# Optimization experiments

Measured on AMD Instinct MI355X. Metric: run time of the kernel, lower is better.

The kernel has to match this reference:

```python
import jax, jax.numpy as jnp
import numpy as np

N_QUBITS = 10
N_LAYERS = 2

# ---- batched statevector simulator helpers (state shape: (B,) + (2,)*n) ----

def _apply1q(state, w, mat):
    # mat: [2,2] complex, same for all batch elements
    s = jnp.moveaxis(state, w + 1, 1)
    s = jnp.einsum('ij,bj...->bi...', mat, s)
    return jnp.moveaxis(s, 1, w + 1)

def _apply1q_b(state, w, mats):
    # mats: [B,2,2] complex, per-batch gate (input-encoding RY)
    s = jnp.moveaxis(state, w + 1, 1)
    s = jnp.einsum('bij,bj...->bi...', mats, s)
    return jnp.moveaxis(s, 1, w + 1)

def _cnot(state, c, t):
    s = jnp.moveaxis(state, (c + 1, t + 1), (1, 2))  # [B,2(ctrl),2(tgt),...]
    s = jnp.concatenate([s[:, :1], jnp.flip(s[:, 1:2], axis=2)], axis=1)
    return jnp.moveaxis(s, (1, 2), (c + 1, t + 1))

def _rz(t):
    p = jnp.exp(-0.5j * t.astype(jnp.complex64))
    z = jnp.zeros((), jnp.complex64)
    return jnp.stack([jnp.stack([p, z]), jnp.stack([z, jnp.conj(p)])])

def _rx(t):
    h = 0.5 * t
    c = jnp.cos(h).astype(jnp.complex64)
    s = jnp.sin(h).astype(jnp.complex64) * (-1j)
    return jnp.stack([jnp.stack([c, s]), jnp.stack([s, c])])

def _ry(t):
    h = 0.5 * t
    c, s = jnp.cos(h), jnp.sin(h)
    return jnp.stack([jnp.stack([c, -s]), jnp.stack([s, c])]).astype(jnp.complex64)

def qlayer(angles, qparams):
    """angles: [B, n_qubits] float -> [B, n_qubits] PauliZ expectations."""
    B = angles.shape[0]
    n = N_QUBITS
    state = jnp.zeros((B,) + (2,) * n, jnp.complex64)
    state = state.at[(slice(None),) + (0,) * n].set(1.0)
    # data-encoding RY with per-batch angles
    half = 0.5 * angles
    c, s = jnp.cos(half), jnp.sin(half)
    for w in range(n):
        row0 = jnp.stack([c[:, w], -s[:, w]], -1)
        row1 = jnp.stack([s[:, w], c[:, w]], -1)
        mats = jnp.stack([row0, row1], 1).astype(jnp.complex64)  # [B,2,2]
        state = _apply1q_b(state, w, mats)
    for l in range(N_LAYERS):
        for w in range(n):
            state = _apply1q(state, w, _rz(qparams[l, w, 0]))
            state = _apply1q(state, w, _rx(qparams[l, w, 1]))
            state = _apply1q(state, w, _ry(qparams[l, w, 2]))
        for w in range(n - 1):
            state = _cnot(state, w, w + 1)
        state = _cnot(state, n - 1, 0)
    probs = jnp.real(state * jnp.conj(state))
    exps = []
    for w in range(n):
        axes = tuple(a for a in range(1, n + 1) if a != w + 1)
        p = jnp.sum(probs, axis=axes)  # [B,2]
        exps.append(p[:, 0] - p[:, 1])
    return jnp.stack(exps, -1)


def setup_inputs() -> dict:
    key = jax.random.key(0)
    ks = jax.random.split(key, 12)
    T, B, D, H = 64, 256, 32, N_QUBITS
    in_dim = D + H
    std = 1.0 / np.sqrt(in_dim)
    inputs = jax.random.normal(ks[0], (T, B, D), jnp.float32)
    qparams = 0.01 * jax.random.normal(ks[1], (N_LAYERS, N_QUBITS, 3), jnp.float32)
    def lin(k1, k2):
        W = jax.random.uniform(k1, (H, in_dim), jnp.float32, -std, std)
        b = jax.random.uniform(k2, (H,), jnp.float32, -std, std)
        return W, b
    W_f, b_f = lin(ks[2], ks[3])
    W_i, b_i = lin(ks[4], ks[5])
    W_g, b_g = lin(ks[6], ks[7])
    W_o, b_o = lin(ks[8], ks[9])
    return dict(inputs=inputs, qparams=qparams, W_f=W_f, b_f=b_f, W_i=W_i, b_i=b_i,
                W_g=W_g, b_g=b_g, W_o=W_o, b_o=b_o)


def reference(inputs, qparams, W_f, b_f, W_i, b_i, W_g, b_g, W_o, b_o):
    T, B, D = inputs.shape
    H = N_QUBITS

    def step(carry, x):
        hx, cx = carry
        comb = jnp.concatenate([x, hx], axis=1)  # [B, D+H]
        pre = jnp.concatenate([
            comb @ W_f.T + b_f,
            comb @ W_i.T + b_i,
            comb @ W_g.T + b_g,
            comb @ W_o.T + b_o,
        ], axis=0)  # [4B, H] -- one fused circuit call for all 4 gates
        q = qlayer(pre, qparams).reshape(4, B, H)
        f = jax.nn.sigmoid(q[0])
        i = jax.nn.sigmoid(q[1])
        g = jnp.tanh(q[2])
        o = jax.nn.sigmoid(q[3])
        cx2 = f * cx + i * g
        hx2 = o * jnp.tanh(cx2)
        return (hx2, cx2), hx2

    hx = jnp.zeros((B, H), jnp.float32)
    cx = jnp.zeros((B, H), jnp.float32)
    (hx, cx), outputs = jax.lax.scan(jax.checkpoint(step), (hx, cx), inputs)
    return outputs, hx, cx
```

## Files before the change

### kernel.cpp

```cpp
#include <hip/hip_runtime.h>

#define TS 64
#define NB 256
#define DI 32
#define NH 10
#define IND 42

typedef float f32x2 __attribute__((ext_vector_type(2)));

#define PKOP2(name, instr, mods) \
__device__ __forceinline__ f32x2 name(f32x2 a, f32x2 b){ \
  f32x2 d; asm(instr " %0, %1, %2 " mods : "=v"(d) : "v"(a), "v"(b)); return d; }
#define PKOP3(name, mods) \
__device__ __forceinline__ f32x2 name(f32x2 a, f32x2 b, f32x2 c){ \
  f32x2 d; asm("v_pk_fma_f32 %0, %1, %2, %3 " mods : "=v"(d) : "v"(a), "v"(b), "v"(c)); return d; }

PKOP2(pk_mul,       "v_pk_mul_f32", "op_sel:[0,0] op_sel_hi:[1,1]")
PKOP2(pk_mul_s0hi,  "v_pk_mul_f32", "op_sel:[1,0] op_sel_hi:[1,1]")
PKOP2(pk_mul_s0lo,  "v_pk_mul_f32", "op_sel:[0,0] op_sel_hi:[0,1]")
PKOP2(pk_mul_s1lo,  "v_pk_mul_f32", "op_sel:[0,0] op_sel_hi:[1,0]")
PKOP2(pk_addsub_ll, "v_pk_add_f32", "op_sel:[0,0] op_sel_hi:[0,0] neg_hi:[0,1]")
PKOP2(pk_addsub_lh, "v_pk_add_f32", "op_sel:[0,1] op_sel_hi:[0,1] neg_hi:[0,1]")
PKOP3(pk_fma_s1lo,  "op_sel:[0,0,0] op_sel_hi:[1,0,1]")
PKOP3(pk_fma_s1hi,  "op_sel:[0,1,0] op_sel_hi:[1,1,1]")
PKOP3(pk_fma_s1swap,"op_sel:[0,1,0] op_sel_hi:[1,0,1]")
PKOP3(pk_fma_am,    "op_sel:[1,1,0] op_sel_hi:[1,0,1] neg_lo:[1,0,0]")
PKOP3(pk_fma_s0lo,  "op_sel:[0,0,0] op_sel_hi:[0,1,1]")
PKOP3(pk_fma_s0hi,  "op_sel:[1,0,0] op_sel_hi:[1,1,1]")

template<int CTRL>
__device__ __forceinline__ float dppx(float v){
  return __int_as_float(__builtin_amdgcn_update_dpp(
      0, __float_as_int(v), CTRL, 0xF, 0xF, true));
}
__device__ __forceinline__ float rl(float v, int lane){
  return __int_as_float(__builtin_amdgcn_readlane(__float_as_int(v), lane));
}
__device__ __forceinline__ f32x2 rl2(f32x2 v, int lane){
  f32x2 r; r.x = rl(v.x, lane); r.y = rl(v.y, lane); return r;
}
__device__ __forceinline__ void pin(float& x){ asm volatile("" : "+v"(x)); }
__device__ __forceinline__ void pinv(f32x2& x){ asm volatile("" : "+v"(x)); }

__device__ __forceinline__ float tanhr(float x){ float e = __expf(2.f*x); return 1.f - 2.f/(e + 1.f); }

__device__ __forceinline__ void mkU(float t1, float t2, float t3, float* dst){
  float c1 = __cosf(0.5f*t1), s1 = __sinf(0.5f*t1);
  float c2 = __cosf(0.5f*t2), s2 = __sinf(0.5f*t2);
  float c3 = __cosf(0.5f*t3), s3 = __sinf(0.5f*t3);
  float A00r =  c2*c1, A00i = -c2*s1;
  float A01r =  s2*s1, A01i = -s2*c1;
  float A10r = -s2*s1, A10i = -s2*c1;
  float A11r =  c2*c1, A11i =  c2*s1;
  dst[0] = c3*A00r - s3*A10r; dst[1] = c3*A00i - s3*A10i;
  dst[2] = c3*A01r - s3*A11r; dst[3] = c3*A01i - s3*A11i;
  dst[4] = s3*A00r + c3*A10r; dst[5] = s3*A00i + c3*A10i;
  dst[6] = s3*A01r + c3*A11r; dst[7] = s3*A01i + c3*A11i;
}

__device__ __forceinline__ float3 qf(float q00, float q11, float q01){
  return make_float3(0.5f*(q00+q11), 0.5f*(q00-q11), 0.5f*q01);
}

__global__ __launch_bounds__(256) __attribute__((amdgpu_waves_per_eu(1, 1)))
void qlstm_kernel(const float* __restrict__ xin,
                  const float* __restrict__ qp,
                  const float* __restrict__ Wf, const float* __restrict__ bfp,
                  const float* __restrict__ Wi, const float* __restrict__ bip,
                  const float* __restrict__ Wg, const float* __restrict__ bgp,
                  const float* __restrict__ Wo, const float* __restrict__ bop,
                  float* __restrict__ out)
{
  __shared__ float lx[TS][DI + 1];
  __shared__ float lwx[4][TS][NH];
  __shared__ __align__(16) float lBw[4][NH][4];
  __shared__ __align__(16) float lq[2][NH][4];
  __shared__ float lhout[TS][NH];

  const int tid  = threadIdx.x;
  const int b    = blockIdx.x;
  const int g    = tid >> 6;
  const int lane = tid & 63;
  const int hq   = lane >> 2;
  const int sg   = lane & 3;
  const int hrow = (lane < NH) ? lane : 0;

  const float* Wsel = (g==0) ? Wf : (g==1) ? Wi : (g==2) ? Wg : Wo;
  const float* bsel = (g==0) ? bfp : (g==1) ? bip : (g==2) ? bgp : bop;

  for (int i = tid; i < TS*DI; i += 256) {
    int tt = i >> 5, d = i & 31;
    lx[tt][d] = xin[(size_t)tt*(NB*DI) + b*DI + d];
  }
  if (lane < NH) {
    float u[8];
    mkU(qp[30 + lane*3 + 0], qp[30 + lane*3 + 1], qp[30 + lane*3 + 2], u);
    float B00 = u[0]*u[0]+u[1]*u[1] - (u[4]*u[4]+u[5]*u[5]);
    float B11 = u[2]*u[2]+u[3]*u[3] - (u[6]*u[6]+u[7]*u[7]);
    float B01r= u[0]*u[2]+u[1]*u[3] - (u[4]*u[6]+u[5]*u[7]);
    float B01i= u[1]*u[2]-u[0]*u[3] - (u[5]*u[6]-u[4]*u[7]);
    *reinterpret_cast<float4*>(&lBw[g][lane][0]) = make_float4(B00,B11,B01r,B01i);
  }
  __syncthreads();

  {
    float acc[NH];
    #pragma unroll
    for (int h = 0; h < NH; h++) acc[h] = bsel[h];
    #pragma unroll
    for (int k = 0; k < DI; k++) {
      float xk = lx[lane][k];
      #pragma unroll
      for (int h = 0; h < NH; h++) acc[h] = fmaf(Wsel[h*IND + k], xk, acc[h]);
    }
    #pragma unroll
    for (int h = 0; h < NH; h++) lwx[g][lane][h] = acc[h];
  }

  float wh[NH];
  #pragma unroll
  for (int j = 0; j < NH; j++) wh[j] = Wsel[hrow*IND + DI + j];

  float3 Qn0, Qn1, Qer, Qei;
  {
    float U1[8];
    mkU(qp[hrow*3+0], qp[hrow*3+1], qp[hrow*3+2], U1);
    float r00r=U1[0], r00i=U1[1], r01r=U1[2], r01i=U1[3];
    float r10r=U1[4], r10i=U1[5], r11r=U1[6], r11i=U1[7];
    float P0r,P0i,P1r,P1i, R0r,R0i,R1r,R1i;
    if (lane == 0) {
      P0r=r00r; P0i=r00i; P1r=r01r; P1i=r01i;
      R0r=r10r; R0i=r10i; R1r=r11r; R1i=r11i;
    } else {
      P0r=0.5f*(r00r+r10r); P0i=0.5f*(r00i+r10i);
      P1r=0.5f*(r01r+r11r); P1i=0.5f*(r01i+r11i);
      R0r=0.5f*(r00r-r10r); R0i=0.5f*(r00i-r10i);
      R1r=0.5f*(r01r-r11r); R1i=0.5f*(r01i-r11i);
    }
    Qn0 = qf(P0r*P0r+P0i*P0i, P1r*P1r+P1i*P1i, 2.f*(P0r*P1r+P0i*P1i));
    Qn1 = qf(R0r*R0r+R0i*R0i, R1r*R1r+R1i*R1i, 2.f*(R0r*R1r+R0i*R1i));
    Qer = qf(R0r*P0r+R0i*P0i, R1r*P1r+R1i*P1i,
             (R0r*P1r+R0i*P1i) + (R1r*P0r+R1i*P0i));
    Qei = qf(R0i*P0r-R0r*P0i, R1i*P1r-R1r*P1i,
             (R0i*P1r-R0r*P1i) + (R1i*P0r-R1r*P0i));
  }
  f32x2 QnA, QnB, QnG, QeA, QeB, QeG;
  QnA.x=Qn0.x; QnA.y=Qn1.x;  QnB.x=Qn0.y; QnB.y=Qn1.y;  QnG.x=Qn0.z; QnG.y=Qn1.z;
  QeA.x=Qer.x; QeA.y=Qei.x;  QeB.x=Qer.y; QeB.y=Qei.y;  QeG.x=Qer.z; QeG.y=Qei.z;

  float4 b0 = *reinterpret_cast<const float4*>(&lBw[g][0][0]);
  if (hq == 0) b0 = make_float4(1.f, 1.f, 0.f, 0.f);
  float k0, k3, ka, kb;
  if      (sg == 0) { k0 = b0.x;  k3 = b0.y;  ka = b0.z; kb = -b0.w; }
  else if (sg == 1) { k0 = b0.z;  k3 = b0.z;  ka = 0.5f*(b0.x + b0.y); kb = 0.f; }
  else if (sg == 2) { k0 = -b0.w; k3 = b0.w;  ka = 0.f;  kb = 0.5f*(b0.y - b0.x); }
  else              { k0 = b0.y;  k3 = b0.x;  ka = b0.z; kb = b0.w; }
  {
    const float gsc = (sg == 0 || sg == 3) ? 0.5f : 1.0f;
    k0 *= gsc; k3 *= gsc; ka *= gsc; kb *= gsc;
  }
  const float ka2 = ka + ka, kb2 = kb + kb;
  f32x2 KA, KB, KC, KD;
  KA.x = k0;   KA.y = k0;
  KB.x = k3;   KB.y = -k3;
  KC.x = ka2;  KC.y = -ka2;
  KD.x = -kb2; KD.y = -kb2;

  f32x2 K1[9], K2[9], K3[9], K4[9];
  #pragma unroll
  for (int w = 1; w <= 9; w++) {
    float4 bb = *reinterpret_cast<const float4*>(&lBw[g][w][0]);
    bool inM = (hq == 0) || (w <= hq);
    float Cp = inM ? (bb.x + bb.y) : 2.f;
    float Cm = inM ? (bb.x - bb.y) : 0.f;
    float Cr2 = inM ? (bb.z + bb.z) : 0.f;
    float Ci2 = inM ? (bb.w + bb.w) : 0.f;
    K1[w-1].x = Cp;        K1[w-1].y = Cm;
    K2[w-1].x = Cm + Cm;   K2[w-1].y = Cp + Cp;
    K3[w-1].x = Cr2;       K3[w-1].y = Ci2;
    K4[w-1].x = -(Ci2+Ci2); K4[w-1].y = Cr2 + Cr2;
  }

  #pragma unroll
  for (int w = 0; w < 9; w++) { pinv(K1[w]); pinv(K2[w]); pinv(K3[w]); pinv(K4[w]); }
  #pragma unroll
  for (int j = 0; j < NH; j++) pin(wh[j]);
  pinv(QnA); pinv(QnB); pinv(QnG); pinv(QeA); pinv(QeB); pinv(QeG);
  pinv(KA); pinv(KB); pinv(KC); pinv(KD);

  const float se = (g == 2) ? -2.f : -1.f;
  const float sa = (g == 2) ?  2.f :  1.f;
  const float sb = (g == 2) ? -1.f :  0.f;

  float cstate = 0.f, hval = 0.f;
  float wxcur = lwx[g][0][hrow];

  for (int t = 0; t < TS; t++) {
    const int tb = t & 1;

    float h0 = rl(hval,0), h1 = rl(hval,1), h2 = rl(hval,2), h3 = rl(hval,3), h4 = rl(hval,4);
    float h5 = rl(hval,5), h6 = rl(hval,6), h7 = rl(hval,7), h8 = rl(hval,8), h9 = rl(hval,9);
    float p0 = fmaf(wh[1], h1, wh[0]*h0);
    float p1 = fmaf(wh[3], h3, wh[2]*h2);
    float p2 = fmaf(wh[5], h5, wh[4]*h4);
    float p3 = fmaf(wh[7], h7, wh[6]*h6);
    float p4 = fmaf(wh[9], h9, wh[8]*h8);
    float pre = wxcur + ((p0 + p1) + (p2 + p3) + p4);

    wxcur = lwx[g][(t+1) & (TS-1)][hrow];

    float th = pre * 0.15915494309189535f;
    f32x2 CS; CS.x = __builtin_amdgcn_cosf(th); CS.y = __builtin_amdgcn_sinf(th);
    f32x2 NP = pk_fma_s1lo(QnB, CS, pk_fma_s1hi(QnG, CS, QnA));
    f32x2 EP = pk_fma_s1lo(QeB, CS, pk_fma_s1hi(QeG, CS, QeA));

    f32x2 V1 = rl2(NP, 0), V2 = rl2(EP, 0);
    f32x2 P1 = pk_fma_s1hi(KB, V1, pk_mul_s1lo(KA, V1));
    f32x2 P2 = pk_fma_s1swap(KD, V2, pk_mul(KC, V2));
    #pragma unroll
    for (int w = 1; w <= 9; w++) {
      f32x2 W1 = rl2(NP, w), W2 = rl2(EP, w);
      f32x2 U  = pk_addsub_ll(P1, P2);
      f32x2 M  = pk_mul(U, W1);
      f32x2 T1 = pk_mul_s0hi(P1, W2);
      f32x2 AB = pk_fma_am(P2, W2, T1);
      f32x2 QS = pk_addsub_lh(M, M);
      f32x2 T2 = pk_mul_s0lo(QS, K1[w-1]);
      P1 = pk_fma_s0lo(AB, K2[w-1], T2);
      f32x2 T3 = pk_mul_s0hi(QS, K3[w-1]);
      P2 = pk_fma_s0hi(AB, K4[w-1], T3);
    }

    float Qv = P1.x, Sv = P1.y, Av = P2.x, Bv = P2.y;
    float QpS = Qv + Sv;
    float QmS = Qv - Sv;
    float t0 = (sg & 1) ? Av  : QpS;
    float t1 = (sg & 1) ? QmS : Bv;
    float Ee = (sg & 2) ? t1 : t0;
    Ee += dppx<0xB1>(Ee);
    Ee += dppx<0x4E>(Ee);
    if ((lane & 3) == 0 && hq < NH) {
      lq[tb][hq][g] = fmaf(sa, 1.f/(1.f + __expf(se*Ee)), sb);
    }
    __syncthreads();

    float4 gates = *reinterpret_cast<const float4*>(&lq[tb][hrow][0]);
    cstate = gates.x*cstate + gates.y*gates.z;
    hval = gates.w*tanhr(cstate);
    if (g == 0 && lane < NH) lhout[t][lane] = hval;
  }

  __syncthreads();
  for (int i = tid; i < TS*NH; i += 256) {
    int tt = i / NH, h = i - tt*NH;
    out[(size_t)tt*(NB*NH) + b*NH + h] = lhout[tt][h];
  }
  if (g == 0 && lane < NH) {
    out[(size_t)TS*NB*NH + b*NH + lane]          = hval;
    out[(size_t)TS*NB*NH + NB*NH + b*NH + lane]  = cstate;
  }
}

extern "C" void kernel_launch(void* const* d_in, const int* in_sizes, int n_in,
                              void* d_out, int out_size, void* d_ws, size_t ws_size,
                              hipStream_t stream) {
  (void)in_sizes; (void)n_in; (void)d_ws; (void)ws_size; (void)out_size;
  qlstm_kernel<<<dim3(NB), dim3(256), 0, stream>>>(
      (const float*)d_in[0], (const float*)d_in[1],
      (const float*)d_in[2], (const float*)d_in[3],
      (const float*)d_in[4], (const float*)d_in[5],
      (const float*)d_in[6], (const float*)d_in[7],
      (const float*)d_in[8], (const float*)d_in[9],
      (float*)d_out);
}
```

Before: 118.2 us.

## Collapse block to single wavefront, one lane per gate-qubit, drop barriers

The block shrinks from four wavefronts (one per gate) to a single 64-lane wavefront in which each 16-lane group handles one gate and each lane one qubit. Per-wire values are exchanged through LDS instead of readlane. Each lane now evaluates all four observable components with two interleaved packed chains, which removes the DPP reduction and the per-step __syncthreads. The x-projection for all four gates runs in each thread before the time loop. The aim is to cut per-step barrier and cross-wave synchronisation latency on the serial recurrence, at the cost of more ALU work per lane and reliance on intra-wave LDS ordering without explicit barriers.

```diff
diff --git a/kernel.cpp b/kernel.cpp
--- a/kernel.cpp
+++ b/kernel.cpp
@@ -15,29 +15,18 @@
 __device__ __forceinline__ f32x2 name(f32x2 a, f32x2 b, f32x2 c){ \
   f32x2 d; asm("v_pk_fma_f32 %0, %1, %2, %3 " mods : "=v"(d) : "v"(a), "v"(b), "v"(c)); return d; }
 
-PKOP2(pk_mul,       "v_pk_mul_f32", "op_sel:[0,0] op_sel_hi:[1,1]")
-PKOP2(pk_mul_s0hi,  "v_pk_mul_f32", "op_sel:[1,0] op_sel_hi:[1,1]")
-PKOP2(pk_mul_s0lo,  "v_pk_mul_f32", "op_sel:[0,0] op_sel_hi:[0,1]")
-PKOP2(pk_mul_s1lo,  "v_pk_mul_f32", "op_sel:[0,0] op_sel_hi:[1,0]")
-PKOP2(pk_addsub_ll, "v_pk_add_f32", "op_sel:[0,0] op_sel_hi:[0,0] neg_hi:[0,1]")
-PKOP2(pk_addsub_lh, "v_pk_add_f32", "op_sel:[0,1] op_sel_hi:[0,1] neg_hi:[0,1]")
-PKOP3(pk_fma_s1lo,  "op_sel:[0,0,0] op_sel_hi:[1,0,1]")
-PKOP3(pk_fma_s1hi,  "op_sel:[0,1,0] op_sel_hi:[1,1,1]")
-PKOP3(pk_fma_s1swap,"op_sel:[0,1,0] op_sel_hi:[1,0,1]")
-PKOP3(pk_fma_am,    "op_sel:[1,1,0] op_sel_hi:[1,0,1] neg_lo:[1,0,0]")
-PKOP3(pk_fma_s0lo,  "op_sel:[0,0,0] op_sel_hi:[0,1,1]")
-PKOP3(pk_fma_s0hi,  "op_sel:[1,0,0] op_sel_hi:[1,1,1]")
-
-template<int CTRL>
-__device__ __forceinline__ float dppx(float v){
-  return __int_as_float(__builtin_amdgcn_update_dpp(
-      0, __float_as_int(v), CTRL, 0xF, 0xF, true));
-}
+PKOP2(pk_add_p,   "v_pk_add_f32", "op_sel:[0,0] op_sel_hi:[1,1]")
+PKOP2(pk_sub_p,   "v_pk_add_f32", "op_sel:[0,0] op_sel_hi:[1,1] neg_lo:[0,1] neg_hi:[0,1]")
+PKOP2(pk_mul_bl,  "v_pk_mul_f32", "op_sel:[0,0] op_sel_hi:[1,0]")
+PKOP2(pk_mul_bh,  "v_pk_mul_f32", "op_sel:[0,1] op_sel_hi:[1,1]")
+PKOP2(pk_mul_bl_na,"v_pk_mul_f32","op_sel:[0,0] op_sel_hi:[1,0] neg_lo:[1,0] neg_hi:[1,0]")
+PKOP3(pk_fma_bl,  "op_sel:[0,0,0] op_sel_hi:[1,0,1]")
+PKOP3(pk_fma_bh,  "op_sel:[0,1,0] op_sel_hi:[1,1,1]")
+PKOP3(pk_fma_bh_na,"op_sel:[0,1,0] op_sel_hi:[1,1,1] neg_lo:[1,0,0] neg_hi:[1,0,0]")
+PKOP3(pk_fma_bl_nac,"op_sel:[0,0,0] op_sel_hi:[1,0,1] neg_lo:[1,0,1] neg_hi:[1,0,1]")
+
 __device__ __forceinline__ float rl(float v, int lane){
   return __int_as_float(__builtin_amdgcn_readlane(__float_as_int(v), lane));
-}
-__device__ __forceinline__ f32x2 rl2(f32x2 v, int lane){
-  f32x2 r; r.x = rl(v.x, lane); r.y = rl(v.y, lane); return r;
 }
 __device__ __forceinline__ void pin(float& x){ asm volatile("" : "+v"(x)); }
 __device__ __forceinline__ void pinv(f32x2& x){ asm volatile("" : "+v"(x)); }
@@ -62,7 +51,31 @@
   return make_float3(0.5f*(q00+q11), 0.5f*(q00-q11), 0.5f*q01);
 }
 
-__global__ __launch_bounds__(256) __attribute__((amdgpu_waves_per_eu(1, 1)))
+__device__ __forceinline__ void wire_step(f32x2& Q, f32x2& S, f32x2& A, f32x2& B,
+                                          f32x2 W1, f32x2 W2,
+                                          f32x2 K1w, f32x2 K3w, f32x2 K5w){
+  f32x2 u0 = pk_add_p(Q, A);
+  f32x2 u3 = pk_sub_p(Q, A);
+  f32x2 m0 = pk_mul_bl(u0, W1);
+  f32x2 m3 = pk_mul_bh(u3, W1);
+  f32x2 t1 = pk_mul_bl(S, W2);
+  f32x2 am = pk_fma_bh_na(B, W2, t1);
+  f32x2 t2 = pk_mul_bh(S, W2);
+  f32x2 bm = pk_fma_bl(B, W2, t2);
+  f32x2 q2 = pk_add_p(m0, m3);
+  f32x2 s2 = pk_sub_p(m0, m3);
+  f32x2 am2 = pk_add_p(am, am);
+  f32x2 t3 = pk_mul_bl(q2, K1w);
+  Q = pk_fma_bh(am2, K1w, t3);
+  f32x2 t4 = pk_mul_bh(q2, K1w);
+  S = pk_fma_bl(am2, K1w, t4);
+  f32x2 t5 = pk_mul_bl_na(bm, K5w);
+  A = pk_fma_bl(s2, K3w, t5);
+  f32x2 t6 = pk_mul_bh(bm, K5w);
+  B = pk_fma_bh(s2, K3w, t6);
+}
+
+__global__ __launch_bounds__(64) __attribute__((amdgpu_waves_per_eu(1, 1)))
 void qlstm_kernel(const float* __restrict__ xin,
                   const float* __restrict__ qp,
                   const float* __restrict__ Wf, const float* __restrict__ bfp,
@@ -73,48 +86,48 @@
 {
   __shared__ float lx[TS][DI + 1];
   __shared__ float lwx[4][TS][NH];
-  __shared__ __align__(16) float lBw[4][NH][4];
-  __shared__ __align__(16) float lq[2][NH][4];
+  __shared__ __align__(16) float lBw[NH][4];
+  __shared__ __align__(16) float4 lvv[4][17];
+  __shared__ __align__(16) float lact[16][4];
   __shared__ float lhout[TS][NH];
 
   const int tid  = threadIdx.x;
   const int b    = blockIdx.x;
-  const int g    = tid >> 6;
-  const int lane = tid & 63;
-  const int hq   = lane >> 2;
-  const int sg   = lane & 3;
-  const int hrow = (lane < NH) ? lane : 0;
+  const int g    = tid >> 4;
+  const int hq   = tid & 15;
+  const int hrow = (hq < NH) ? hq : 0;
 
   const float* Wsel = (g==0) ? Wf : (g==1) ? Wi : (g==2) ? Wg : Wo;
-  const float* bsel = (g==0) ? bfp : (g==1) ? bip : (g==2) ? bgp : bop;
-
-  for (int i = tid; i < TS*DI; i += 256) {
+
+  for (int i = tid; i < TS*DI; i += 64) {
     int tt = i >> 5, d = i & 31;
     lx[tt][d] = xin[(size_t)tt*(NB*DI) + b*DI + d];
   }
-  if (lane < NH) {
+  if (tid < NH) {
     float u[8];
-    mkU(qp[30 + lane*3 + 0], qp[30 + lane*3 + 1], qp[30 + lane*3 + 2], u);
+    mkU(qp[30 + tid*3 + 0], qp[30 + tid*3 + 1], qp[30 + tid*3 + 2], u);
     float B00 = u[0]*u[0]+u[1]*u[1] - (u[4]*u[4]+u[5]*u[5]);
     float B11 = u[2]*u[2]+u[3]*u[3] - (u[6]*u[6]+u[7]*u[7]);
     float B01r= u[0]*u[2]+u[1]*u[3] - (u[4]*u[6]+u[5]*u[7]);
     float B01i= u[1]*u[2]-u[0]*u[3] - (u[5]*u[6]-u[4]*u[7]);
-    *reinterpret_cast<float4*>(&lBw[g][lane][0]) = make_float4(B00,B11,B01r,B01i);
-  }
-  __syncthreads();
-
-  {
+    *reinterpret_cast<float4*>(&lBw[tid][0]) = make_float4(B00,B11,B01r,B01i);
+  }
+
+  #pragma unroll
+  for (int gg = 0; gg < 4; gg++) {
+    const float* W  = (gg==0) ? Wf : (gg==1) ? Wi : (gg==2) ? Wg : Wo;
+    const float* bv = (gg==0) ? bfp : (gg==1) ? bip : (gg==2) ? bgp : bop;
     float acc[NH];
     #pragma unroll
-    for (int h = 0; h < NH; h++) acc[h] = bsel[h];
+    for (int h = 0; h < NH; h++) acc[h] = bv[h];
     #pragma unroll
     for (int k = 0; k < DI; k++) {
-      float xk = lx[lane][k];
+      float xk = lx[tid][k];
       #pragma unroll
-      for (int h = 0; h < NH; h++) acc[h] = fmaf(Wsel[h*IND + k], xk, acc[h]);
+      for (int h = 0; h < NH; h++) acc[h] = fmaf(W[h*IND + k], xk, acc[h]);
     }
     #pragma unroll
-    for (int h = 0; h < NH; h++) lwx[g][lane][h] = acc[h];
+    for (int h = 0; h < NH; h++) lwx[gg][tid][h] = acc[h];
   }
 
   float wh[NH];
@@ -128,7 +141,7 @@
     float r00r=U1[0], r00i=U1[1], r01r=U1[2], r01i=U1[3];
     float r10r=U1[4], r10i=U1[5], r11r=U1[6], r11i=U1[7];
     float P0r,P0i,P1r,P1i, R0r,R0i,R1r,R1i;
-    if (lane == 0) {
+    if (hq == 0) {
       P0r=r00r; P0i=r00i; P1r=r01r; P1i=r01i;
       R0r=r10r; R0i=r10i; R1r=r11r; R1i=r11i;
     } else {
@@ -148,45 +161,41 @@
   QnA.x=Qn0.x; QnA.y=Qn1.x;  QnB.x=Qn0.y; QnB.y=Qn1.y;  QnG.x=Qn0.z; QnG.y=Qn1.z;
   QeA.x=Qer.x; QeA.y=Qei.x;  QeB.x=Qer.y; QeB.y=Qei.y;  QeG.x=Qer.z; QeG.y=Qei.z;
 
-  float4 b0 = *reinterpret_cast<const float4*>(&lBw[g][0][0]);
+  float4 b0 = *reinterpret_cast<const float4*>(&lBw[0][0]);
   if (hq == 0) b0 = make_float4(1.f, 1.f, 0.f, 0.f);
-  float k0, k3, ka, kb;
-  if      (sg == 0) { k0 = b0.x;  k3 = b0.y;  ka = b0.z; kb = -b0.w; }
-  else if (sg == 1) { k0 = b0.z;  k3 = b0.z;  ka = 0.5f*(b0.x + b0.y); kb = 0.f; }
-  else if (sg == 2) { k0 = -b0.w; k3 = b0.w;  ka = 0.f;  kb = 0.5f*(b0.y - b0.x); }
-  else              { k0 = b0.y;  k3 = b0.x;  ka = b0.z; kb = b0.w; }
+  f32x2 k0a, k0b, k3a, k3b, ka2a, ka2b, kb2a, kb2b;
   {
-    const float gsc = (sg == 0 || sg == 3) ? 0.5f : 1.0f;
-    k0 *= gsc; k3 *= gsc; ka *= gsc; kb *= gsc;
-  }
-  const float ka2 = ka + ka, kb2 = kb + kb;
-  f32x2 KA, KB, KC, KD;
-  KA.x = k0;   KA.y = k0;
-  KB.x = k3;   KB.y = -k3;
-  KC.x = ka2;  KC.y = -ka2;
-  KD.x = -kb2; KD.y = -kb2;
-
-  f32x2 K1[9], K2[9], K3[9], K4[9];
+    float k0_0 = 0.5f*b0.x, k3_0 = 0.5f*b0.y, ka_0 = 0.5f*b0.z, kb_0 = -0.5f*b0.w;
+    float k0_1 = b0.z,      k3_1 = b0.z,      ka_1 = 0.5f*(b0.x+b0.y), kb_1 = 0.f;
+    float k0_2 = -b0.w,     k3_2 = b0.w,      ka_2 = 0.f, kb_2 = 0.5f*(b0.y-b0.x);
+    float k0_3 = 0.5f*b0.y, k3_3 = 0.5f*b0.x, ka_3 = 0.5f*b0.z, kb_3 = 0.5f*b0.w;
+    k0a.x=k0_0; k0a.y=k0_1;   k0b.x=k0_2; k0b.y=k0_3;
+    k3a.x=k3_0; k3a.y=k3_1;   k3b.x=k3_2; k3b.y=k3_3;
+    ka2a.x=ka_0+ka_0; ka2a.y=ka_1+ka_1;  ka2b.x=ka_2+ka_2; ka2b.y=ka_3+ka_3;
+    kb2a.x=kb_0+kb_0; kb2a.y=kb_1+kb_1;  kb2b.x=kb_2+kb_2; kb2b.y=kb_3+kb_3;
+  }
+
+  f32x2 K1c[9], K3c[9], K5c[9];
   #pragma unroll
   for (int w = 1; w <= 9; w++) {
-    float4 bb = *reinterpret_cast<const float4*>(&lBw[g][w][0]);
+    float4 bb = *reinterpret_cast<const float4*>(&lBw[w][0]);
     bool inM = (hq == 0) || (w <= hq);
-    float Cp = inM ? (bb.x + bb.y) : 2.f;
-    float Cm = inM ? (bb.x - bb.y) : 0.f;
+    float Cp  = inM ? (bb.x + bb.y) : 2.f;
+    float Cm  = inM ? (bb.x - bb.y) : 0.f;
     float Cr2 = inM ? (bb.z + bb.z) : 0.f;
     float Ci2 = inM ? (bb.w + bb.w) : 0.f;
-    K1[w-1].x = Cp;        K1[w-1].y = Cm;
-    K2[w-1].x = Cm + Cm;   K2[w-1].y = Cp + Cp;
-    K3[w-1].x = Cr2;       K3[w-1].y = Ci2;
-    K4[w-1].x = -(Ci2+Ci2); K4[w-1].y = Cr2 + Cr2;
-  }
-
-  #pragma unroll
-  for (int w = 0; w < 9; w++) { pinv(K1[w]); pinv(K2[w]); pinv(K3[w]); pinv(K4[w]); }
+    K1c[w-1].x = Cp;        K1c[w-1].y = Cm;
+    K3c[w-1].x = Cr2;       K3c[w-1].y = Ci2;
+    K5c[w-1].x = Ci2 + Ci2; K5c[w-1].y = Cr2 + Cr2;
+  }
+
+  #pragma unroll
+  for (int w = 0; w < 9; w++) { pinv(K1c[w]); pinv(K3c[w]); pinv(K5c[w]); }
   #pragma unroll
   for (int j = 0; j < NH; j++) pin(wh[j]);
   pinv(QnA); pinv(QnB); pinv(QnG); pinv(QeA); pinv(QeB); pinv(QeG);
-  pinv(KA); pinv(KB); pinv(KC); pinv(KD);
+  pinv(k0a); pinv(k0b); pinv(k3a); pinv(k3b);
+  pinv(ka2a); pinv(ka2b); pinv(kb2a); pinv(kb2b);
 
   const float se = (g == 2) ? -2.f : -1.f;
   const float sa = (g == 2) ?  2.f :  1.f;
@@ -196,8 +205,6 @@
   float wxcur = lwx[g][0][hrow];
 
   for (int t = 0; t < TS; t++) {
-    const int tb = t & 1;
-
     float h0 = rl(hval,0), h1 = rl(hval,1), h2 = rl(hval,2), h3 = rl(hval,3), h4 = rl(hval,4);
     float h5 = rl(hval,5), h6 = rl(hval,6), h7 = rl(hval,7), h8 = rl(hval,8), h9 = rl(hval,9);
     float p0 = fmaf(wh[1], h1, wh[0]*h0);
@@ -211,53 +218,54 @@
 
     float th = pre * 0.15915494309189535f;
     f32x2 CS; CS.x = __builtin_amdgcn_cosf(th); CS.y = __builtin_amdgcn_sinf(th);
-    f32x2 NP = pk_fma_s1lo(QnB, CS, pk_fma_s1hi(QnG, CS, QnA));
-    f32x2 EP = pk_fma_s1lo(QeB, CS, pk_fma_s1hi(QeG, CS, QeA));
-
-    f32x2 V1 = rl2(NP, 0), V2 = rl2(EP, 0);
-    f32x2 P1 = pk_fma_s1hi(KB, V1, pk_mul_s1lo(KA, V1));
-    f32x2 P2 = pk_fma_s1swap(KD, V2, pk_mul(KC, V2));
+    f32x2 NP = pk_fma_bl(QnB, CS, pk_fma_bh(QnG, CS, QnA));
+    f32x2 EP = pk_fma_bl(QeB, CS, pk_fma_bh(QeG, CS, QeA));
+    float4 vs; vs.x = NP.x; vs.y = NP.y; vs.z = EP.x; vs.w = EP.y;
+    lvv[g][hq] = vs;
+
+    float4 v0 = lvv[g][0];
+    f32x2 W1, W2;
+    W1.x = v0.x; W1.y = v0.y; W2.x = v0.z; W2.y = v0.w;
+    f32x2 ta = pk_mul_bl(k0a, W1);
+    f32x2 Qa = pk_fma_bh(k3a, W1, ta);
+    f32x2 Sa = pk_fma_bh_na(k3a, W1, ta);
+    f32x2 ua = pk_mul_bl(ka2a, W2);
+    f32x2 Aa = pk_fma_bh_na(kb2a, W2, ua);
+    f32x2 va = pk_mul_bh(ka2a, W2);
+    f32x2 Ba = pk_fma_bl_nac(kb2a, W2, va);
+    f32x2 tb = pk_mul_bl(k0b, W1);
+    f32x2 Qb = pk_fma_bh(k3b, W1, tb);
+    f32x2 Sb = pk_fma_bh_na(k3b, W1, tb);
+    f32x2 ub = pk_mul_bl(ka2b, W2);
+    f32x2 Ab = pk_fma_bh_na(kb2b, W2, ub);
+    f32x2 vb = pk_mul_bh(ka2b, W2);
+    f32x2 Bb = pk_fma_bl_nac(kb2b, W2, vb);
     #pragma unroll
     for (int w = 1; w <= 9; w++) {
-      f32x2 W1 = rl2(NP, w), W2 = rl2(EP, w);
-      f32x2 U  = pk_addsub_ll(P1, P2);
-      f32x2 M  = pk_mul(U, W1);
-      f32x2 T1 = pk_mul_s0hi(P1, W2);
-      f32x2 AB = pk_fma_am(P2, W2, T1);
-      f32x2 QS = pk_addsub_lh(M, M);
-      f32x2 T2 = pk_mul_s0lo(QS, K1[w-1]);
-      P1 = pk_fma_s0lo(AB, K2[w-1], T2);
-      f32x2 T3 = pk_mul_s0hi(QS, K3[w-1]);
-      P2 = pk_fma_s0hi(AB, K4[w-1], T3);
+      float4 vv = lvv[g][w];
+      W1.x = vv.x; W1.y = vv.y; W2.x = vv.z; W2.y = vv.w;
+      wire_step(Qa, Sa, Aa, Ba, W1, W2, K1c[w-1], K3c[w-1], K5c[w-1]);
+      wire_step(Qb, Sb, Ab, Bb, W1, W2, K1c[w-1], K3c[w-1], K5c[w-1]);
     }
 
-    float Qv = P1.x, Sv = P1.y, Av = P2.x, Bv = P2.y;
-    float QpS = Qv + Sv;
-    float QmS = Qv - Sv;
-    float t0 = (sg & 1) ? Av  : QpS;
-    float t1 = (sg & 1) ? QmS : Bv;
-    float Ee = (sg & 2) ? t1 : t0;
-    Ee += dppx<0xB1>(Ee);
-    Ee += dppx<0x4E>(Ee);
-    if ((lane & 3) == 0 && hq < NH) {
-      lq[tb][hq][g] = fmaf(sa, 1.f/(1.f + __expf(se*Ee)), sb);
-    }
-    __syncthreads();
-
-    float4 gates = *reinterpret_cast<const float4*>(&lq[tb][hrow][0]);
+    float Ee = ((Qa.x + Sa.x) + Aa.y) + (Bb.x + (Qb.y - Sb.y));
+
+    float act = fmaf(sa, 1.f/(1.f + __expf(se*Ee)), sb);
+    lact[hq][g] = act;
+    float4 gates = *reinterpret_cast<const float4*>(&lact[hq][0]);
+
     cstate = gates.x*cstate + gates.y*gates.z;
     hval = gates.w*tanhr(cstate);
-    if (g == 0 && lane < NH) lhout[t][lane] = hval;
-  }
-
-  __syncthreads();
-  for (int i = tid; i < TS*NH; i += 256) {
+    if (tid < NH) lhout[t][tid] = hval;
+  }
+
+  for (int i = tid; i < TS*NH; i += 64) {
     int tt = i / NH, h = i - tt*NH;
     out[(size_t)tt*(NB*NH) + b*NH + h] = lhout[tt][h];
   }
-  if (g == 0 && lane < NH) {
-    out[(size_t)TS*NB*NH + b*NH + lane]          = hval;
-    out[(size_t)TS*NB*NH + NB*NH + b*NH + lane]  = cstate;
+  if (tid < NH) {
+    out[(size_t)TS*NB*NH + b*NH + tid]          = hval;
+    out[(size_t)TS*NB*NH + NB*NH + b*NH + tid]  = cstate;
   }
 }
 
@@ -265,7 +273,7 @@
                               void* d_out, int out_size, void* d_ws, size_t ws_size,
                               hipStream_t stream) {
   (void)in_sizes; (void)n_in; (void)d_ws; (void)ws_size; (void)out_size;
-  qlstm_kernel<<<dim3(NB), dim3(256), 0, stream>>>(
+  qlstm_kernel<<<dim3(NB), dim3(64), 0, stream>>>(
       (const float*)d_in[0], (const float*)d_in[1],
       (const float*)d_in[2], (const float*)d_in[3],
       (const float*)d_in[4], (const float*)d_in[5],
```

After: 154.8 us. 1.31x slower.

## Process two batch elements per block using packed-float lanes

Applied to the files above, without the earlier changes.

Each block now handles two batch elements, carrying both through the recurrence in the two halves of packed f32x2 registers, and the grid is halved to NB/2 blocks. The per-wire circuit contraction is rewritten as a new packed wire_step2 routine that operates across the two batch elements instead of across real/imag pairs. The aim is to spread the latency-bound sequential per-timestep chain (readlanes, barriers, transcendentals) over two samples per block. The cost is fewer blocks (128 on a device with many CUs), more instructions per step, and the packed asm is now volatile, which limits scheduling.

```diff
diff --git a/kernel.cpp b/kernel.cpp
--- a/kernel.cpp
+++ b/kernel.cpp
@@ -10,23 +10,23 @@
 
 #define PKOP2(name, instr, mods) \
 __device__ __forceinline__ f32x2 name(f32x2 a, f32x2 b){ \
-  f32x2 d; asm(instr " %0, %1, %2 " mods : "=v"(d) : "v"(a), "v"(b)); return d; }
+  f32x2 d; asm volatile(instr " %0, %1, %2 " mods : "=v"(d) : "v"(a), "v"(b)); return d; }
 #define PKOP3(name, mods) \
 __device__ __forceinline__ f32x2 name(f32x2 a, f32x2 b, f32x2 c){ \
-  f32x2 d; asm("v_pk_fma_f32 %0, %1, %2, %3 " mods : "=v"(d) : "v"(a), "v"(b), "v"(c)); return d; }
-
-PKOP2(pk_mul,       "v_pk_mul_f32", "op_sel:[0,0] op_sel_hi:[1,1]")
-PKOP2(pk_mul_s0hi,  "v_pk_mul_f32", "op_sel:[1,0] op_sel_hi:[1,1]")
-PKOP2(pk_mul_s0lo,  "v_pk_mul_f32", "op_sel:[0,0] op_sel_hi:[0,1]")
-PKOP2(pk_mul_s1lo,  "v_pk_mul_f32", "op_sel:[0,0] op_sel_hi:[1,0]")
-PKOP2(pk_addsub_ll, "v_pk_add_f32", "op_sel:[0,0] op_sel_hi:[0,0] neg_hi:[0,1]")
-PKOP2(pk_addsub_lh, "v_pk_add_f32", "op_sel:[0,1] op_sel_hi:[0,1] neg_hi:[0,1]")
-PKOP3(pk_fma_s1lo,  "op_sel:[0,0,0] op_sel_hi:[1,0,1]")
-PKOP3(pk_fma_s1hi,  "op_sel:[0,1,0] op_sel_hi:[1,1,1]")
-PKOP3(pk_fma_s1swap,"op_sel:[0,1,0] op_sel_hi:[1,0,1]")
-PKOP3(pk_fma_am,    "op_sel:[1,1,0] op_sel_hi:[1,0,1] neg_lo:[1,0,0]")
-PKOP3(pk_fma_s0lo,  "op_sel:[0,0,0] op_sel_hi:[0,1,1]")
-PKOP3(pk_fma_s0hi,  "op_sel:[1,0,0] op_sel_hi:[1,1,1]")
+  f32x2 d; asm volatile("v_pk_fma_f32 %0, %1, %2, %3 " mods : "=v"(d) : "v"(a), "v"(b), "v"(c)); return d; }
+
+PKOP2(pk_add_p,    "v_pk_add_f32", "op_sel:[0,0] op_sel_hi:[1,1]")
+PKOP2(pk_sub_p,    "v_pk_add_f32", "op_sel:[0,0] op_sel_hi:[1,1] neg_lo:[0,1] neg_hi:[0,1]")
+PKOP2(pk_mul_pp,   "v_pk_mul_f32", "op_sel:[0,0] op_sel_hi:[1,1]")
+PKOP2(pk_mul_bl,   "v_pk_mul_f32", "op_sel:[0,0] op_sel_hi:[1,0]")
+PKOP2(pk_mul_bh,   "v_pk_mul_f32", "op_sel:[0,1] op_sel_hi:[1,1]")
+PKOP2(pk_mul_bh_na,"v_pk_mul_f32", "op_sel:[0,1] op_sel_hi:[1,1] neg_lo:[1,0] neg_hi:[1,0]")
+PKOP3(pk_fma_pp,   "op_sel:[0,0,0] op_sel_hi:[1,1,1]")
+PKOP3(pk_fma_na,   "op_sel:[0,0,0] op_sel_hi:[1,1,1] neg_lo:[1,0,0] neg_hi:[1,0,0]")
+PKOP3(pk_fma_bl,   "op_sel:[0,0,0] op_sel_hi:[1,0,1]")
+PKOP3(pk_fma_bh,   "op_sel:[0,1,0] op_sel_hi:[1,1,1]")
+PKOP3(pk_fma_bh_na,"op_sel:[0,1,0] op_sel_hi:[1,1,1] neg_lo:[1,0,0] neg_hi:[1,0,0]")
+PKOP3(pk_fma_bh_nac,"op_sel:[0,1,0] op_sel_hi:[1,1,1] neg_lo:[1,0,1] neg_hi:[1,0,1]")
 
 template<int CTRL>
 __device__ __forceinline__ float dppx(float v){
@@ -39,8 +39,6 @@
 __device__ __forceinline__ f32x2 rl2(f32x2 v, int lane){
   f32x2 r; r.x = rl(v.x, lane); r.y = rl(v.y, lane); return r;
 }
-__device__ __forceinline__ void pin(float& x){ asm volatile("" : "+v"(x)); }
-__device__ __forceinline__ void pinv(f32x2& x){ asm volatile("" : "+v"(x)); }
 
 __device__ __forceinline__ float tanhr(float x){ float e = __expf(2.f*x); return 1.f - 2.f/(e + 1.f); }
 
@@ -62,6 +60,29 @@
   return make_float3(0.5f*(q00+q11), 0.5f*(q00-q11), 0.5f*q01);
 }
 
+__device__ __forceinline__ void wire_step2(f32x2& Q, f32x2& S, f32x2& A, f32x2& B,
+    f32x2 vx, f32x2 vy, f32x2 vr, f32x2 vi, f32x2 Kp, f32x2 Kq, f32x2 Kr){
+  f32x2 u0 = pk_add_p(Q, A);
+  f32x2 u3 = pk_sub_p(Q, A);
+  f32x2 m0 = pk_mul_pp(u0, vx);
+  f32x2 m3 = pk_mul_pp(u3, vy);
+  f32x2 t1 = pk_mul_pp(S, vr);
+  f32x2 am = pk_fma_na(B, vi, t1);
+  f32x2 t2 = pk_mul_pp(S, vi);
+  f32x2 bm = pk_fma_pp(B, vr, t2);
+  f32x2 q2 = pk_add_p(m0, m3);
+  f32x2 s2 = pk_sub_p(m0, m3);
+  f32x2 am2 = pk_add_p(am, am);
+  f32x2 t3 = pk_mul_bl(q2, Kp);
+  Q = pk_fma_bh(am2, Kp, t3);
+  f32x2 t4 = pk_mul_bh(q2, Kp);
+  S = pk_fma_bl(am2, Kp, t4);
+  f32x2 t5 = pk_mul_bh_na(bm, Kq);
+  A = pk_fma_bl(s2, Kq, t5);
+  f32x2 t6 = pk_mul_bh(bm, Kr);
+  B = pk_fma_bl(s2, Kr, t6);
+}
+
 __global__ __launch_bounds__(256) __attribute__((amdgpu_waves_per_eu(1, 1)))
 void qlstm_kernel(const float* __restrict__ xin,
                   const float* __restrict__ qp,
@@ -71,14 +92,14 @@
                   const float* __restrict__ Wo, const float* __restrict__ bop,
                   float* __restrict__ out)
 {
-  __shared__ float lx[TS][DI + 1];
-  __shared__ float lwx[4][TS][NH];
+  __shared__ float lx[2][TS][DI + 1];
+  __shared__ __align__(8) f32x2 lwx[4][TS][NH];
   __shared__ __align__(16) float lBw[4][NH][4];
-  __shared__ __align__(16) float lq[2][NH][4];
-  __shared__ float lhout[TS][NH];
+  __shared__ __align__(16) f32x2 lq[2][NH][5];
+  __shared__ __align__(8) f32x2 lhout[TS][NH];
 
   const int tid  = threadIdx.x;
-  const int b    = blockIdx.x;
+  const int bA   = blockIdx.x * 2;
   const int g    = tid >> 6;
   const int lane = tid & 63;
   const int hq   = lane >> 2;
@@ -88,9 +109,9 @@
   const float* Wsel = (g==0) ? Wf : (g==1) ? Wi : (g==2) ? Wg : Wo;
   const float* bsel = (g==0) ? bfp : (g==1) ? bip : (g==2) ? bgp : bop;
 
-  for (int i = tid; i < TS*DI; i += 256) {
-    int tt = i >> 5, d = i & 31;
-    lx[tt][d] = xin[(size_t)tt*(NB*DI) + b*DI + d];
+  for (int i = tid; i < 2*TS*DI; i += 256) {
+    int ss = i >> 11, r = i & 2047, tt = r >> 5, d = r & 31;
+    lx[ss][tt][d] = xin[(size_t)tt*(NB*DI) + (size_t)(bA + ss)*DI + d];
   }
   if (lane < NH) {
     float u[8];
@@ -104,22 +125,32 @@
   __syncthreads();
 
   {
-    float acc[NH];
+    float accA[NH], accB[NH];
     #pragma unroll
-    for (int h = 0; h < NH; h++) acc[h] = bsel[h];
+    for (int h = 0; h < NH; h++) { accA[h] = bsel[h]; accB[h] = bsel[h]; }
     #pragma unroll
     for (int k = 0; k < DI; k++) {
-      float xk = lx[lane][k];
+      float xkA = lx[0][lane][k], xkB = lx[1][lane][k];
       #pragma unroll
-      for (int h = 0; h < NH; h++) acc[h] = fmaf(Wsel[h*IND + k], xk, acc[h]);
+      for (int h = 0; h < NH; h++) {
+        float w = Wsel[h*IND + k];
+        accA[h] = fmaf(w, xkA, accA[h]);
+        accB[h] = fmaf(w, xkB, accB[h]);
+      }
     }
     #pragma unroll
-    for (int h = 0; h < NH; h++) lwx[g][lane][h] = acc[h];
-  }
-
-  float wh[NH];
+    for (int h = 0; h < NH; h++) {
+      f32x2 p; p.x = accA[h]; p.y = accB[h];
+      lwx[g][lane][h] = p;
+    }
+  }
+
+  f32x2 whp[NH];
   #pragma unroll
-  for (int j = 0; j < NH; j++) wh[j] = Wsel[hrow*IND + DI + j];
+  for (int j = 0; j < NH; j++) {
+    float w = Wsel[hrow*IND + DI + j];
+    whp[j].x = w; whp[j].y = w;
+  }
 
   float3 Qn0, Qn1, Qer, Qei;
   {
@@ -144,9 +175,11 @@
     Qei = qf(R0i*P0r-R0r*P0i, R1i*P1r-R1r*P1i,
              (R0i*P1r-R0r*P1i) + (R1i*P0r-R1r*P0i));
   }
-  f32x2 QnA, QnB, QnG, QeA, QeB, QeG;
-  QnA.x=Qn0.x; QnA.y=Qn1.x;  QnB.x=Qn0.y; QnB.y=Qn1.y;  QnG.x=Qn0.z; QnG.y=Qn1.z;
-  QeA.x=Qer.x; QeA.y=Qei.x;  QeB.x=Qer.y; QeB.y=Qei.y;  QeG.x=Qer.z; QeG.y=Qei.z;
+  f32x2 BGn0, An0, BGn1, An1, BGer, Aer, BGei, Aei;
+  BGn0.x=Qn0.y; BGn0.y=Qn0.z; An0.x=Qn0.x; An0.y=Qn0.x;
+  BGn1.x=Qn1.y; BGn1.y=Qn1.z; An1.x=Qn1.x; An1.y=Qn1.x;
+  BGer.x=Qer.y; BGer.y=Qer.z; Aer.x=Qer.x; Aer.y=Qer.x;
+  BGei.x=Qei.y; BGei.y=Qei.z; Aei.x=Qei.x; Aei.y=Qei.x;
 
   float4 b0 = *reinterpret_cast<const float4*>(&lBw[g][0][0]);
   if (hq == 0) b0 = make_float4(1.f, 1.f, 0.f, 0.f);
@@ -159,105 +192,112 @@
     const float gsc = (sg == 0 || sg == 3) ? 0.5f : 1.0f;
     k0 *= gsc; k3 *= gsc; ka *= gsc; kb *= gsc;
   }
-  const float ka2 = ka + ka, kb2 = kb + kb;
-  f32x2 KA, KB, KC, KD;
-  KA.x = k0;   KA.y = k0;
-  KB.x = k3;   KB.y = -k3;
-  KC.x = ka2;  KC.y = -ka2;
-  KD.x = -kb2; KD.y = -kb2;
-
-  f32x2 K1[9], K2[9], K3[9], K4[9];
+  f32x2 KK1, KK2;
+  KK1.x = k0;      KK1.y = k3;
+  KK2.x = ka + ka; KK2.y = kb + kb;
+
+  f32x2 Kp[9], Kq[9], Kr[9];
   #pragma unroll
   for (int w = 1; w <= 9; w++) {
     float4 bb = *reinterpret_cast<const float4*>(&lBw[g][w][0]);
     bool inM = (hq == 0) || (w <= hq);
-    float Cp = inM ? (bb.x + bb.y) : 2.f;
-    float Cm = inM ? (bb.x - bb.y) : 0.f;
+    float Cpv = inM ? (bb.x + bb.y) : 2.f;
+    float Cmv = inM ? (bb.x - bb.y) : 0.f;
     float Cr2 = inM ? (bb.z + bb.z) : 0.f;
     float Ci2 = inM ? (bb.w + bb.w) : 0.f;
-    K1[w-1].x = Cp;        K1[w-1].y = Cm;
-    K2[w-1].x = Cm + Cm;   K2[w-1].y = Cp + Cp;
-    K3[w-1].x = Cr2;       K3[w-1].y = Ci2;
-    K4[w-1].x = -(Ci2+Ci2); K4[w-1].y = Cr2 + Cr2;
-  }
-
-  #pragma unroll
-  for (int w = 0; w < 9; w++) { pinv(K1[w]); pinv(K2[w]); pinv(K3[w]); pinv(K4[w]); }
-  #pragma unroll
-  for (int j = 0; j < NH; j++) pin(wh[j]);
-  pinv(QnA); pinv(QnB); pinv(QnG); pinv(QeA); pinv(QeB); pinv(QeG);
-  pinv(KA); pinv(KB); pinv(KC); pinv(KD);
+    Kp[w-1].x = Cpv;       Kp[w-1].y = Cmv;
+    Kq[w-1].x = Cr2;       Kq[w-1].y = Ci2 + Ci2;
+    Kr[w-1].x = Ci2;       Kr[w-1].y = Cr2 + Cr2;
+  }
 
   const float se = (g == 2) ? -2.f : -1.f;
   const float sa = (g == 2) ?  2.f :  1.f;
   const float sb = (g == 2) ? -1.f :  0.f;
 
-  float cstate = 0.f, hval = 0.f;
-  float wxcur = lwx[g][0][hrow];
+  f32x2 cstate; cstate.x = 0.f; cstate.y = 0.f;
+  f32x2 hval;   hval.x = 0.f;   hval.y = 0.f;
+  f32x2 wxcur = lwx[g][0][hrow];
 
   for (int t = 0; t < TS; t++) {
     const int tb = t & 1;
 
-    float h0 = rl(hval,0), h1 = rl(hval,1), h2 = rl(hval,2), h3 = rl(hval,3), h4 = rl(hval,4);
-    float h5 = rl(hval,5), h6 = rl(hval,6), h7 = rl(hval,7), h8 = rl(hval,8), h9 = rl(hval,9);
-    float p0 = fmaf(wh[1], h1, wh[0]*h0);
-    float p1 = fmaf(wh[3], h3, wh[2]*h2);
-    float p2 = fmaf(wh[5], h5, wh[4]*h4);
-    float p3 = fmaf(wh[7], h7, wh[6]*h6);
-    float p4 = fmaf(wh[9], h9, wh[8]*h8);
-    float pre = wxcur + ((p0 + p1) + (p2 + p3) + p4);
+    f32x2 h0p = rl2(hval,0), h1p = rl2(hval,1), h2p = rl2(hval,2), h3p = rl2(hval,3), h4p = rl2(hval,4);
+    f32x2 h5p = rl2(hval,5), h6p = rl2(hval,6), h7p = rl2(hval,7), h8p = rl2(hval,8), h9p = rl2(hval,9);
+    f32x2 p0 = pk_fma_bl(h1p, whp[1], pk_mul_bl(h0p, whp[0]));
+    f32x2 p1 = pk_fma_bl(h3p, whp[3], pk_mul_bl(h2p, whp[2]));
+    f32x2 p2 = pk_fma_bl(h5p, whp[5], pk_mul_bl(h4p, whp[4]));
+    f32x2 p3 = pk_fma_bl(h7p, whp[7], pk_mul_bl(h6p, whp[6]));
+    f32x2 p4 = pk_fma_bl(h9p, whp[9], pk_mul_bl(h8p, whp[8]));
+    f32x2 pre = pk_add_p(wxcur,
+                  pk_add_p(pk_add_p(pk_add_p(p0, p1), pk_add_p(p2, p3)), p4));
 
     wxcur = lwx[g][(t+1) & (TS-1)][hrow];
 
-    float th = pre * 0.15915494309189535f;
-    f32x2 CS; CS.x = __builtin_amdgcn_cosf(th); CS.y = __builtin_amdgcn_sinf(th);
-    f32x2 NP = pk_fma_s1lo(QnB, CS, pk_fma_s1hi(QnG, CS, QnA));
-    f32x2 EP = pk_fma_s1lo(QeB, CS, pk_fma_s1hi(QeG, CS, QeA));
-
-    f32x2 V1 = rl2(NP, 0), V2 = rl2(EP, 0);
-    f32x2 P1 = pk_fma_s1hi(KB, V1, pk_mul_s1lo(KA, V1));
-    f32x2 P2 = pk_fma_s1swap(KD, V2, pk_mul(KC, V2));
+    float thA = pre.x * 0.15915494309189535f;
+    float thB = pre.y * 0.15915494309189535f;
+    f32x2 Cc, Ss;
+    Cc.x = __builtin_amdgcn_cosf(thA); Cc.y = __builtin_amdgcn_cosf(thB);
+    Ss.x = __builtin_amdgcn_sinf(thA); Ss.y = __builtin_amdgcn_sinf(thB);
+    f32x2 n0p = pk_fma_bl(Cc, BGn0, pk_fma_bh(Ss, BGn0, An0));
+    f32x2 n1p = pk_fma_bl(Cc, BGn1, pk_fma_bh(Ss, BGn1, An1));
+    f32x2 erp = pk_fma_bl(Cc, BGer, pk_fma_bh(Ss, BGer, Aer));
+    f32x2 eip = pk_fma_bl(Cc, BGei, pk_fma_bh(Ss, BGei, Aei));
+
+    f32x2 vx0 = rl2(n0p,0), vy0 = rl2(n1p,0), vr0 = rl2(erp,0), vi0 = rl2(eip,0);
+    f32x2 t1i = pk_mul_bl(vx0, KK1);
+    f32x2 Qc  = pk_fma_bh(vy0, KK1, t1i);
+    f32x2 Sc  = pk_fma_bh_na(vy0, KK1, t1i);
+    f32x2 t2i = pk_mul_bl(vr0, KK2);
+    f32x2 Ac  = pk_fma_bh_na(vi0, KK2, t2i);
+    f32x2 t3i = pk_mul_bl(vi0, KK2);
+    f32x2 Bc  = pk_fma_bh_nac(vr0, KK2, t3i);
     #pragma unroll
     for (int w = 1; w <= 9; w++) {
-      f32x2 W1 = rl2(NP, w), W2 = rl2(EP, w);
-      f32x2 U  = pk_addsub_ll(P1, P2);
-      f32x2 M  = pk_mul(U, W1);
-      f32x2 T1 = pk_mul_s0hi(P1, W2);
-      f32x2 AB = pk_fma_am(P2, W2, T1);
-      f32x2 QS = pk_addsub_lh(M, M);
-      f32x2 T2 = pk_mul_s0lo(QS, K1[w-1]);
-      P1 = pk_fma_s0lo(AB, K2[w-1], T2);
-      f32x2 T3 = pk_mul_s0hi(QS, K3[w-1]);
-      P2 = pk_fma_s0hi(AB, K4[w-1], T3);
-    }
-
-    float Qv = P1.x, Sv = P1.y, Av = P2.x, Bv = P2.y;
-    float QpS = Qv + Sv;
-    float QmS = Qv - Sv;
-    float t0 = (sg & 1) ? Av  : QpS;
-    float t1 = (sg & 1) ? QmS : Bv;
-    float Ee = (sg & 2) ? t1 : t0;
-    Ee += dppx<0xB1>(Ee);
-    Ee += dppx<0x4E>(Ee);
+      f32x2 vxw = rl2(n0p, w), vyw = rl2(n1p, w);
+      f32x2 vrw = rl2(erp, w), viw = rl2(eip, w);
+      wire_step2(Qc, Sc, Ac, Bc, vxw, vyw, vrw, viw, Kp[w-1], Kq[w-1], Kr[w-1]);
+    }
+
+    float QpSx = Qc.x + Sc.x, QpSy = Qc.y + Sc.y;
+    float QmSx = Qc.x - Sc.x, QmSy = Qc.y - Sc.y;
+    float t0x = (sg & 1) ? Ac.x  : QpSx;
+    float t0y = (sg & 1) ? Ac.y  : QpSy;
+    float t1x = (sg & 1) ? QmSx : Bc.x;
+    float t1y = (sg & 1) ? QmSy : Bc.y;
+    float ex = (sg & 2) ? t1x : t0x;
+    float ey = (sg & 2) ? t1y : t0y;
+    ex += dppx<0xB1>(ex); ex += dppx<0x4E>(ex);
+    ey += dppx<0xB1>(ey); ey += dppx<0x4E>(ey);
     if ((lane & 3) == 0 && hq < NH) {
-      lq[tb][hq][g] = fmaf(sa, 1.f/(1.f + __expf(se*Ee)), sb);
+      f32x2 act;
+      act.x = fmaf(sa, 1.f/(1.f + __expf(se*ex)), sb);
+      act.y = fmaf(sa, 1.f/(1.f + __expf(se*ey)), sb);
+      lq[tb][hq][g] = act;
     }
     __syncthreads();
 
-    float4 gates = *reinterpret_cast<const float4*>(&lq[tb][hrow][0]);
-    cstate = gates.x*cstate + gates.y*gates.z;
-    hval = gates.w*tanhr(cstate);
+    f32x2 gf = lq[tb][hrow][0];
+    f32x2 gi = lq[tb][hrow][1];
+    f32x2 gg = lq[tb][hrow][2];
+    f32x2 go = lq[tb][hrow][3];
+    cstate = pk_fma_pp(gf, cstate, pk_mul_pp(gi, gg));
+    f32x2 tc; tc.x = tanhr(cstate.x); tc.y = tanhr(cstate.y);
+    hval = pk_mul_pp(go, tc);
     if (g == 0 && lane < NH) lhout[t][lane] = hval;
   }
 
   __syncthreads();
   for (int i = tid; i < TS*NH; i += 256) {
     int tt = i / NH, h = i - tt*NH;
-    out[(size_t)tt*(NB*NH) + b*NH + h] = lhout[tt][h];
+    f32x2 hv = lhout[tt][h];
+    out[(size_t)tt*(NB*NH) + (size_t)bA*NH + h]       = hv.x;
+    out[(size_t)tt*(NB*NH) + (size_t)(bA+1)*NH + h]   = hv.y;
   }
   if (g == 0 && lane < NH) {
-    out[(size_t)TS*NB*NH + b*NH + lane]          = hval;
-    out[(size_t)TS*NB*NH + NB*NH + b*NH + lane]  = cstate;
+    out[(size_t)TS*NB*NH + (size_t)bA*NH + lane]              = hval.x;
+    out[(size_t)TS*NB*NH + (size_t)(bA+1)*NH + lane]          = hval.y;
+    out[(size_t)TS*NB*NH + NB*NH + (size_t)bA*NH + lane]      = cstate.x;
+    out[(size_t)TS*NB*NH + NB*NH + (size_t)(bA+1)*NH + lane]  = cstate.y;
   }
 }
 
@@ -265,7 +305,7 @@
                               void* d_out, int out_size, void* d_ws, size_t ws_size,
                               hipStream_t stream) {
   (void)in_sizes; (void)n_in; (void)d_ws; (void)ws_size; (void)out_size;
-  qlstm_kernel<<<dim3(NB), dim3(256), 0, stream>>>(
+  qlstm_kernel<<<dim3(NB/2), dim3(256), 0, stream>>>(
       (const float*)d_in[0], (const float*)d_in[1],
       (const float*)d_in[2], (const float*)d_in[3],
       (const float*)d_in[4], (const float*)d_in[5],
```

Result: slower. 149.4 us (+26.4%).
